# Optimization experiments

Measured on AMD Instinct MI355X. Metric: run time of the kernel, lower is better.

Reference implementation:

```python
import jax, jax.numpy as jnp
import numpy as np

N = 50000          # num nodes
E = 800000         # num edges
D = 128            # dim_in == embed_dim
MAX_NODES = 4      # hard-coded in SortConv.__init__
EPS = 1e-5


def setup_inputs() -> dict:
    key = jax.random.key(0)
    ks = jax.random.split(key, 16)
    inp = {
        'x': jax.random.normal(ks[0], (N, D), jnp.float32),
        'edge_index': jax.random.randint(ks[1], (2, E), 0, N, jnp.int32),
    }
    for i in range(2):
        o = 2 + 6 * i
        W = jax.random.normal(ks[o], (D, D), jnp.float32) * (2.0 / (D + D)) ** 0.5
        W = W / jnp.linalg.norm(W, axis=1, keepdims=True)   # reset_parameters row-normalization
        inp[f'W{i}'] = W
        inp[f'b{i}'] = jnp.zeros((D,), jnp.float32)
        inp[f'cw{i}'] = jax.random.normal(ks[o + 1], (MAX_NODES,), jnp.float32) * (2.0 / (MAX_NODES + 1)) ** 0.5
        inp[f'cb{i}'] = jnp.zeros((1,), jnp.float32)
        inp[f'a{i}'] = jax.random.uniform(ks[o + 2], (1,), jnp.float32, -1.0, 1.0)  # LinearCombination scalar
        inp[f'g{i}'] = jnp.ones((D,), jnp.float32)
        inp[f'be{i}'] = jnp.zeros((D,), jnp.float32)
        inp[f'blank{i}'] = jnp.zeros((D,), jnp.float32)      # learnable blank vector
    return inp


def sort_conv(x, edge_index, blank, W, b, cw, cb, a):
    n, d = x.shape
    e = edge_index.shape[1]
    src, dst = edge_index[0], edge_index[1]
    msgs = x[src]                                            # [E, D] raw messages (lin_project not applied to messages)
    order = jnp.argsort(dst)                                 # stable sort by destination (index_sort)
    dst_s = dst[order]
    counts = jax.ops.segment_sum(jnp.ones((e,), jnp.int32), dst, num_segments=n + 1)
    starts = jnp.concatenate([jnp.zeros((1,), jnp.int32), jnp.cumsum(counts)[:-1].astype(jnp.int32)])
    pos = jnp.arange(e, dtype=jnp.int32) - starts[dst_s]     # rank within each neighborhood
    slot = jnp.where(pos < MAX_NODES, pos, MAX_NODES)        # overflow edges -> trash slot (to_dense_batch truncation)
    dense = jnp.zeros((n + 1, MAX_NODES + 1, d), x.dtype).at[dst_s, slot].set(msgs[order])
    mask = jnp.zeros((n + 1, MAX_NODES + 1), bool).at[dst_s, slot].set(True)
    dense, mask = dense[:, :MAX_NODES], mask[:, :MAX_NODES]  # [N+1, 4, D], [N+1, 4]
    blank_p = W @ blank + b                                  # lin_project applied only to blank vector
    filled = dense + (~mask)[..., None].astype(x.dtype) * blank_p
    srt = jnp.sort(filled, axis=1)                           # per-feature sort over neighbor slots
    out = jnp.einsum('nmd,m->nd', srt, cw) + cb              # vector collapse: Linear(max_nodes, 1)
    node_out, blank_new = out[:-1], out[-1]                  # last row = all-blank graph -> new blank
    return a * x + node_out, a * blank + blank_new           # LinearCombination combine (num_repeats=1)


def batch_norm(h, g, be):
    mu = h.mean(0)
    var = h.var(0)
    return (h - mu) / jnp.sqrt(var + EPS) * g + be


def reference(x, edge_index, W0, b0, cw0, cb0, a0, g0, be0, blank0,
              W1, b1, cw1, cb1, a1, g1, be1, blank1):
    layers = [(W0, b0, cw0, cb0, a0, g0, be0, blank0),
              (W1, b1, cw1, cb1, a1, g1, be1, blank1)]
    for (W, b, cw, cb, a, g, be, blank) in layers:
        h, _ = sort_conv(x, edge_index, blank, W, b, cw, cb, a)
        h = batch_norm(h, g, be)
        x = x + h                                            # residual connection
    return x
```

## Files before the change

kernel.cpp:

```cpp
#include <hip/hip_runtime.h>
#include <climits>

constexpr int N_NODES = 50000;
constexpr int N_EDGES = 800000;
constexpr int DIM     = 128;
constexpr int DIM4    = DIM / 4;
constexpr float BN_EPS = 1e-5f;

constexpr int EMPTY = 0x7F7F7F7F;

constexpr int NC = 16;
constexpr int EC = 16;
constexpr int NODES_PER_NC = N_NODES / NC;
constexpr int EDGES_PER_EC = N_EDGES / EC;
constexpr int E4_PER_EC    = EDGES_PER_EC / 4;

constexpr int NODES_PER_ITER  = 8;
constexpr int CONV_ITERS      = 2;
constexpr int NODES_PER_BLOCK = NODES_PER_ITER * CONV_ITERS;
constexpr int CONV_GRID = N_NODES / NODES_PER_BLOCK;

constexpr int NBUCKETS = 64;

__device__ inline float4 f4min(float4 a, float4 b) {
    return make_float4(fminf(a.x,b.x), fminf(a.y,b.y), fminf(a.z,b.z), fminf(a.w,b.w));
}
__device__ inline float4 f4max(float4 a, float4 b) {
    return make_float4(fmaxf(a.x,b.x), fmaxf(a.y,b.y), fmaxf(a.z,b.z), fmaxf(a.w,b.w));
}
__device__ inline float4 f4add(float4 a, float4 b) {
    return make_float4(a.x+b.x, a.y+b.y, a.z+b.z, a.w+b.w);
}
__device__ inline float4 f4fma(float s, float4 v, float4 acc) {
    return make_float4(fmaf(s,v.x,acc.x), fmaf(s,v.y,acc.y), fmaf(s,v.z,acc.z), fmaf(s,v.w,acc.w));
}

__global__ __launch_bounds__(256)
void select_stageA_kernel(const int* __restrict__ dst,
                          int* __restrict__ tables) {
    __shared__ int slot[NODES_PER_NC * 4];
    const int nc = blockIdx.x & (NC - 1);
    const int ec = blockIdx.x >> 4;
    const int t  = threadIdx.x;

    for (int i = t; i < NODES_PER_NC * 4; i += 256) slot[i] = EMPTY;
    __syncthreads();

    const int r0 = nc * NODES_PER_NC;
    const int4* __restrict__ dst4 = (const int4*)dst;
    const int base4 = ec * E4_PER_EC;
    for (int i = t; i < E4_PER_EC; i += 256) {
        const int4 d = dst4[base4 + i];
        const int ebase = 4 * (base4 + i);
        #define TRY_INS(comp, off) {                                        \
            unsigned n_ = (unsigned)((comp) - r0);                          \
            if (n_ < (unsigned)NODES_PER_NC) {                              \
                int cur_ = ebase + (off);                                   \
                _Pragma("unroll")                                           \
                for (int j_ = 0; j_ < 4; ++j_) {                            \
                    int old_ = atomicMin(&slot[4 * n_ + j_], cur_);         \
                    if (old_ == EMPTY) break;                               \
                    cur_ = max(cur_, old_);                                 \
                } } }
        TRY_INS(d.x, 0); TRY_INS(d.y, 1); TRY_INS(d.z, 2); TRY_INS(d.w, 3);
        #undef TRY_INS
    }
    __syncthreads();

    int4* __restrict__ out = (int4*)tables + (size_t)ec * N_NODES + r0;
    const int4* __restrict__ sl4 = (const int4*)slot;
    for (int n = t; n < NODES_PER_NC; n += 256) out[n] = sl4[n];
}

__global__ void select_stageB_kernel(const int* __restrict__ tables,
                                     const int* __restrict__ src,
                                     int4* __restrict__ srcs4) {
    int v = blockIdx.x * blockDim.x + threadIdx.x;
    if (v >= N_NODES) return;

    int b0 = EMPTY, b1 = EMPTY, b2 = EMPTY, b3 = EMPTY;
    #pragma unroll
    for (int ec = 0; ec < EC; ++ec) {
        const int4 c = ((const int4*)tables)[(size_t)ec * N_NODES + v];
        #define INS(val) {                                          \
            int x_ = (val);                                         \
            if (x_ < b3) { b3 = x_;                                 \
                int tm;                                             \
                if (b3 < b2) { tm = b2; b2 = b3; b3 = tm; }         \
                if (b2 < b1) { tm = b1; b1 = b2; b2 = tm; }         \
                if (b1 < b0) { tm = b0; b0 = b1; b1 = tm; } } }
        INS(c.x); INS(c.y); INS(c.z); INS(c.w);
        #undef INS
    }
    int4 o;
    o.x = (b0 < N_EDGES) ? src[b0] : -1;
    o.y = (b1 < N_EDGES) ? src[b1] : -1;
    o.z = (b2 < N_EDGES) ? src[b2] : -1;
    o.w = (b3 < N_EDGES) ? src[b3] : -1;
    srcs4[v] = o;
}

__global__ void blank_proj_kernel(const float* __restrict__ W0, const float* __restrict__ b0,
                                  const float* __restrict__ bl0,
                                  const float* __restrict__ W1, const float* __restrict__ b1,
                                  const float* __restrict__ bl1,
                                  float* __restrict__ bp) {
    int l = blockIdx.x;
    int d = threadIdx.x;
    const float* W  = l ? W1  : W0;
    const float* b  = l ? b1  : b0;
    const float* bl = l ? bl1 : bl0;
    float s = 0.f;
    #pragma unroll 8
    for (int j = 0; j < DIM; ++j) s += W[d * DIM + j] * bl[j];
    bp[l * DIM + d] = s + b[d];
}

__global__ __launch_bounds__(256)
void conv_stats_kernel(const float* __restrict__ x,
                       const int4* __restrict__ srcs4,
                       const float* __restrict__ bp,
                       const float* __restrict__ cw,
                       const float* __restrict__ cb,
                       const float* __restrict__ a,
                       float* __restrict__ h,
                       float* __restrict__ stats_part) {
    const int t    = threadIdx.x;
    const int d4   = t & (DIM4 - 1);
    const int nsub = t >> 5;

    const float4* __restrict__ x4 = (const float4*)x;
    float4*       __restrict__ h4 = (float4*)h;

    const float aa = a[0];
    const float c0 = cw[0], c1 = cw[1], c2 = cw[2], c3 = cw[3];
    const float cbv = cb[0];
    const float4 bpv = ((const float4*)bp)[d4];

    const int v0 = blockIdx.x * NODES_PER_BLOCK + nsub;
    const int v1 = v0 + NODES_PER_ITER;

    const int4 s0 = srcs4[v0];
    const int4 s1 = srcs4[v1];

    float4 g00 = x4[(size_t)max(s0.x, 0) * DIM4 + d4];
    float4 g01 = x4[(size_t)max(s0.y, 0) * DIM4 + d4];
    float4 g02 = x4[(size_t)max(s0.z, 0) * DIM4 + d4];
    float4 g03 = x4[(size_t)max(s0.w, 0) * DIM4 + d4];
    float4 g10 = x4[(size_t)max(s1.x, 0) * DIM4 + d4];
    float4 g11 = x4[(size_t)max(s1.y, 0) * DIM4 + d4];
    float4 g12 = x4[(size_t)max(s1.z, 0) * DIM4 + d4];
    float4 g13 = x4[(size_t)max(s1.w, 0) * DIM4 + d4];
    float4 xv0 = x4[(size_t)v0 * DIM4 + d4];
    float4 xv1 = x4[(size_t)v1 * DIM4 + d4];

    float4 s  = make_float4(0.f, 0.f, 0.f, 0.f);
    float4 s2 = make_float4(0.f, 0.f, 0.f, 0.f);

    #define CSWAP4(p, q) { float4 lo = f4min(p, q); float4 hi = f4max(p, q); p = lo; q = hi; }
    {
        float4 m0 = (s0.x >= 0) ? g00 : bpv;
        float4 m1 = (s0.y >= 0) ? g01 : bpv;
        float4 m2 = (s0.z >= 0) ? g02 : bpv;
        float4 m3 = (s0.w >= 0) ? g03 : bpv;
        CSWAP4(m0, m1); CSWAP4(m2, m3); CSWAP4(m0, m2); CSWAP4(m1, m3); CSWAP4(m1, m2);
        float4 hv = make_float4(cbv, cbv, cbv, cbv);
        hv = f4fma(c0, m0, hv);
        hv = f4fma(c1, m1, hv);
        hv = f4fma(c2, m2, hv);
        hv = f4fma(c3, m3, hv);
        hv = f4fma(aa, xv0, hv);
        h4[(size_t)v0 * DIM4 + d4] = hv;
        s  = f4add(s, hv);
        s2 = f4add(s2, make_float4(hv.x*hv.x, hv.y*hv.y, hv.z*hv.z, hv.w*hv.w));
    }
    {
        float4 m0 = (s1.x >= 0) ? g10 : bpv;
        float4 m1 = (s1.y >= 0) ? g11 : bpv;
        float4 m2 = (s1.z >= 0) ? g12 : bpv;
        float4 m3 = (s1.w >= 0) ? g13 : bpv;
        CSWAP4(m0, m1); CSWAP4(m2, m3); CSWAP4(m0, m2); CSWAP4(m1, m3); CSWAP4(m1, m2);
        float4 hv = make_float4(cbv, cbv, cbv, cbv);
        hv = f4fma(c0, m0, hv);
        hv = f4fma(c1, m1, hv);
        hv = f4fma(c2, m2, hv);
        hv = f4fma(c3, m3, hv);
        hv = f4fma(aa, xv1, hv);
        h4[(size_t)v1 * DIM4 + d4] = hv;
        s  = f4add(s, hv);
        s2 = f4add(s2, make_float4(hv.x*hv.x, hv.y*hv.y, hv.z*hv.z, hv.w*hv.w));
    }
    #undef CSWAP4

    s.x  += __shfl_down(s.x, 32);  s.y  += __shfl_down(s.y, 32);
    s.z  += __shfl_down(s.z, 32);  s.w  += __shfl_down(s.w, 32);
    s2.x += __shfl_down(s2.x, 32); s2.y += __shfl_down(s2.y, 32);
    s2.z += __shfl_down(s2.z, 32); s2.w += __shfl_down(s2.w, 32);

    __shared__ float4 ls[4][32];
    __shared__ float4 ls2[4][32];
    const int wave = t >> 6;
    const int lane = t & 63;
    if (lane < 32) { ls[wave][lane] = s; ls2[wave][lane] = s2; }
    __syncthreads();
    if (t < 32) {
        float* bucket = stats_part + (size_t)(blockIdx.x & (NBUCKETS - 1)) * 256;
        float4 fs  = f4add(f4add(ls[0][t],  ls[1][t]),  f4add(ls[2][t],  ls[3][t]));
        float4 fs2 = f4add(f4add(ls2[0][t], ls2[1][t]), f4add(ls2[2][t], ls2[3][t]));
        atomicAdd(&bucket[4*t + 0], fs.x);
        atomicAdd(&bucket[4*t + 1], fs.y);
        atomicAdd(&bucket[4*t + 2], fs.z);
        atomicAdd(&bucket[4*t + 3], fs.w);
        atomicAdd(&bucket[DIM + 4*t + 0], fs2.x);
        atomicAdd(&bucket[DIM + 4*t + 1], fs2.y);
        atomicAdd(&bucket[DIM + 4*t + 2], fs2.z);
        atomicAdd(&bucket[DIM + 4*t + 3], fs2.w);
    }
}

__global__ void reduce_finalize_kernel(const float* __restrict__ stats_part,
                                       float* __restrict__ final) {
    __shared__ float acc[256];
    int t = threadIdx.x;
    float s = 0.f;
    #pragma unroll 8
    for (int k = 0; k < NBUCKETS; ++k) s += stats_part[k * 256 + t];
    acc[t] = s;
    __syncthreads();
    if (t < 128) {
        constexpr float invN = 1.0f / (float)N_NODES;
        float mu = acc[t] * invN;
        float iv = rsqrtf(acc[128 + t] * invN - mu * mu + BN_EPS);
        final[t]       = mu;
        final[128 + t] = iv;
    }
}

__global__ void bn_apply_kernel(const float* __restrict__ xin,
                                const float* __restrict__ h,
                                const float* __restrict__ final,
                                const float* __restrict__ g,
                                const float* __restrict__ be,
                                float* __restrict__ xout) {
    int idx = blockIdx.x * blockDim.x + threadIdx.x;
    constexpr int TOTAL4 = N_NODES * DIM4;
    if (idx >= TOTAL4) return;
    int d4 = idx & (DIM4 - 1);

    float4 mu = ((const float4*)final)[d4];
    float4 iv = ((const float4*)(final + DIM))[d4];
    float4 hv = ((const float4*)h)[idx];
    float4 xv = ((const float4*)xin)[idx];
    float4 gv = ((const float4*)g)[d4];
    float4 bv = ((const float4*)be)[d4];

    float4 o;
    o.x = xv.x + (hv.x - mu.x) * iv.x * gv.x + bv.x;
    o.y = xv.y + (hv.y - mu.y) * iv.y * gv.y + bv.y;
    o.z = xv.z + (hv.z - mu.z) * iv.z * gv.z + bv.z;
    o.w = xv.w + (hv.w - mu.w) * iv.w * gv.w + bv.w;
    ((float4*)xout)[idx] = o;
}

extern "C" void kernel_launch(void* const* d_in, const int* in_sizes, int n_in,
                              void* d_out, int out_size, void* d_ws, size_t ws_size,
                              hipStream_t stream) {
    const float* x0  = (const float*)d_in[0];
    const int*   ei  = (const int*)d_in[1];
    const int*   src = ei;
    const int*   dst = ei + N_EDGES;

    const float* W[2]; const float* b[2]; const float* cw[2]; const float* cb[2];
    const float* a[2]; const float* g[2]; const float* be[2]; const float* blank[2];
    for (int i = 0; i < 2; ++i) {
        int o = 2 + 8 * i;
        W[i]     = (const float*)d_in[o + 0];
        b[i]     = (const float*)d_in[o + 1];
        cw[i]    = (const float*)d_in[o + 2];
        cb[i]    = (const float*)d_in[o + 3];
        a[i]     = (const float*)d_in[o + 4];
        g[i]     = (const float*)d_in[o + 5];
        be[i]    = (const float*)d_in[o + 6];
        blank[i] = (const float*)d_in[o + 7];
    }

    char* ws = (char*)d_ws;
    int*   srcs       = (int*)ws;
    float* h          = (float*)(srcs + 4 * N_NODES);
    int*   tables     = (int*)h;
    float* stats_part = h + (size_t)N_NODES * DIM;
    float* final_     = stats_part + 2 * NBUCKETS * 256;
    float* bp         = final_ + 512;

    float* xout = (float*)d_out;

    hipMemsetAsync(stats_part, 0, 2 * NBUCKETS * 256 * sizeof(float), stream);

    select_stageA_kernel<<<NC * EC, 256, 0, stream>>>(dst, tables);
    select_stageB_kernel<<<(N_NODES + 255) / 256, 256, 0, stream>>>(
        tables, src, (int4*)srcs);

    blank_proj_kernel<<<2, DIM, 0, stream>>>(W[0], b[0], blank[0],
                                             W[1], b[1], blank[1], bp);

    for (int l = 0; l < 2; ++l) {
        const float* xin = (l == 0) ? x0 : xout;
        float* sp = stats_part + (size_t)l * NBUCKETS * 256;
        conv_stats_kernel<<<CONV_GRID, 256, 0, stream>>>(
            xin, (const int4*)srcs, bp + l * DIM, cw[l], cb[l], a[l], h, sp);
        reduce_finalize_kernel<<<1, 256, 0, stream>>>(sp, final_ + l * 256);
        bn_apply_kernel<<<(N_NODES * DIM4 + 255) / 256, 256, 0, stream>>>(
            xin, h, final_ + l * 256, g[l], be[l], xout);
    }
}
```

Before: 237.4 us.

## Fuse memset and blank projection into merge kernel, widen selection blocks

Folds the stats zeroing memset and the blank-vector projection kernel into the stage-B merge kernel as extra blocks, which removes two launches from the stream. Stage-A selection blocks grow from 256 to 1024 threads so more threads work on each shared-memory slot table. Stage-B also skips a table row early when its smallest entry cannot beat the current fourth-best. The larger blocks may lower occupancy and add contention on the shared-memory atomics.

```diff
diff --git a/kernel.cpp b/kernel.cpp
--- a/kernel.cpp
+++ b/kernel.cpp
@@ -14,6 +14,7 @@
 constexpr int NODES_PER_NC = N_NODES / NC;
 constexpr int EDGES_PER_EC = N_EDGES / EC;
 constexpr int E4_PER_EC    = EDGES_PER_EC / 4;
+constexpr int SEL_THREADS  = 1024;
 
 constexpr int NODES_PER_ITER  = 8;
 constexpr int CONV_ITERS      = 2;
@@ -21,6 +22,7 @@
 constexpr int CONV_GRID = N_NODES / NODES_PER_BLOCK;
 
 constexpr int NBUCKETS = 64;
+constexpr int NB_MERGE = (N_NODES + 255) / 256;
 
 __device__ inline float4 f4min(float4 a, float4 b) {
     return make_float4(fminf(a.x,b.x), fminf(a.y,b.y), fminf(a.z,b.z), fminf(a.w,b.w));
@@ -35,7 +37,7 @@
     return make_float4(fmaf(s,v.x,acc.x), fmaf(s,v.y,acc.y), fmaf(s,v.z,acc.z), fmaf(s,v.w,acc.w));
 }
 
-__global__ __launch_bounds__(256)
+__global__ __launch_bounds__(SEL_THREADS)
 void select_stageA_kernel(const int* __restrict__ dst,
                           int* __restrict__ tables) {
     __shared__ int slot[NODES_PER_NC * 4];
@@ -43,13 +45,13 @@
     const int ec = blockIdx.x >> 4;
     const int t  = threadIdx.x;
 
-    for (int i = t; i < NODES_PER_NC * 4; i += 256) slot[i] = EMPTY;
+    for (int i = t; i < NODES_PER_NC * 4; i += SEL_THREADS) slot[i] = EMPTY;
     __syncthreads();
 
     const int r0 = nc * NODES_PER_NC;
     const int4* __restrict__ dst4 = (const int4*)dst;
     const int base4 = ec * E4_PER_EC;
-    for (int i = t; i < E4_PER_EC; i += 256) {
+    for (int i = t; i < E4_PER_EC; i += SEL_THREADS) {
         const int4 d = dst4[base4 + i];
         const int ebase = 4 * (base4 + i);
         #define TRY_INS(comp, off) {                                        \
@@ -69,51 +71,62 @@
 
     int4* __restrict__ out = (int4*)tables + (size_t)ec * N_NODES + r0;
     const int4* __restrict__ sl4 = (const int4*)slot;
-    for (int n = t; n < NODES_PER_NC; n += 256) out[n] = sl4[n];
-}
-
-__global__ void select_stageB_kernel(const int* __restrict__ tables,
-                                     const int* __restrict__ src,
-                                     int4* __restrict__ srcs4) {
-    int v = blockIdx.x * blockDim.x + threadIdx.x;
+    for (int n = t; n < NODES_PER_NC; n += SEL_THREADS) out[n] = sl4[n];
+}
+
+__global__ __launch_bounds__(256)
+void select_stageB_kernel(const int* __restrict__ tables,
+                          const int* __restrict__ src,
+                          int4* __restrict__ srcs4,
+                          float* __restrict__ stats_part,
+                          const float* __restrict__ W0, const float* __restrict__ b0,
+                          const float* __restrict__ bl0,
+                          const float* __restrict__ W1, const float* __restrict__ b1,
+                          const float* __restrict__ bl1,
+                          float* __restrict__ bp) {
+    const int t = threadIdx.x;
+
+    if (blockIdx.x >= NB_MERGE) {
+        if (t < DIM) {
+            int l = blockIdx.x - NB_MERGE;
+            const float* W  = l ? W1  : W0;
+            const float* b  = l ? b1  : b0;
+            const float* bl = l ? bl1 : bl0;
+            float s = 0.f;
+            #pragma unroll 8
+            for (int j = 0; j < DIM; ++j) s += W[t * DIM + j] * bl[j];
+            bp[l * DIM + t] = s + b[t];
+        }
+        return;
+    }
+
+    const int gid = blockIdx.x * 256 + t;
+    if (gid < 2 * NBUCKETS * 256) stats_part[gid] = 0.f;
+
+    const int v = gid;
     if (v >= N_NODES) return;
 
-    int b0 = EMPTY, b1 = EMPTY, b2 = EMPTY, b3 = EMPTY;
+    int b0_ = EMPTY, b1_ = EMPTY, b2_ = EMPTY, b3_ = EMPTY;
     #pragma unroll
     for (int ec = 0; ec < EC; ++ec) {
         const int4 c = ((const int4*)tables)[(size_t)ec * N_NODES + v];
+        if (c.x >= b3_) continue;
         #define INS(val) {                                          \
             int x_ = (val);                                         \
-            if (x_ < b3) { b3 = x_;                                 \
+            if (x_ < b3_) { b3_ = x_;                               \
                 int tm;                                             \
-                if (b3 < b2) { tm = b2; b2 = b3; b3 = tm; }         \
-                if (b2 < b1) { tm = b1; b1 = b2; b2 = tm; }         \
-                if (b1 < b0) { tm = b0; b0 = b1; b1 = tm; } } }
+                if (b3_ < b2_) { tm = b2_; b2_ = b3_; b3_ = tm; }   \
+                if (b2_ < b1_) { tm = b1_; b1_ = b2_; b2_ = tm; }   \
+                if (b1_ < b0_) { tm = b0_; b0_ = b1_; b1_ = tm; } } }
         INS(c.x); INS(c.y); INS(c.z); INS(c.w);
         #undef INS
     }
     int4 o;
-    o.x = (b0 < N_EDGES) ? src[b0] : -1;
-    o.y = (b1 < N_EDGES) ? src[b1] : -1;
-    o.z = (b2 < N_EDGES) ? src[b2] : -1;
-    o.w = (b3 < N_EDGES) ? src[b3] : -1;
+    o.x = (b0_ < N_EDGES) ? src[b0_] : -1;
+    o.y = (b1_ < N_EDGES) ? src[b1_] : -1;
+    o.z = (b2_ < N_EDGES) ? src[b2_] : -1;
+    o.w = (b3_ < N_EDGES) ? src[b3_] : -1;
     srcs4[v] = o;
-}
-
-__global__ void blank_proj_kernel(const float* __restrict__ W0, const float* __restrict__ b0,
-                                  const float* __restrict__ bl0,
-                                  const float* __restrict__ W1, const float* __restrict__ b1,
-                                  const float* __restrict__ bl1,
-                                  float* __restrict__ bp) {
-    int l = blockIdx.x;
-    int d = threadIdx.x;
-    const float* W  = l ? W1  : W0;
-    const float* b  = l ? b1  : b0;
-    const float* bl = l ? bl1 : bl0;
-    float s = 0.f;
-    #pragma unroll 8
-    for (int j = 0; j < DIM; ++j) s += W[d * DIM + j] * bl[j];
-    bp[l * DIM + d] = s + b[d];
 }
 
 __global__ __launch_bounds__(256)
@@ -294,14 +307,10 @@
 
     float* xout = (float*)d_out;
 
-    hipMemsetAsync(stats_part, 0, 2 * NBUCKETS * 256 * sizeof(float), stream);
-
-    select_stageA_kernel<<<NC * EC, 256, 0, stream>>>(dst, tables);
-    select_stageB_kernel<<<(N_NODES + 255) / 256, 256, 0, stream>>>(
-        tables, src, (int4*)srcs);
-
-    blank_proj_kernel<<<2, DIM, 0, stream>>>(W[0], b[0], blank[0],
-                                             W[1], b[1], blank[1], bp);
+    select_stageA_kernel<<<NC * EC, SEL_THREADS, 0, stream>>>(dst, tables);
+    select_stageB_kernel<<<NB_MERGE + 2, 256, 0, stream>>>(
+        tables, src, (int4*)srcs, stats_part,
+        W[0], b[0], blank[0], W[1], b[1], blank[1], bp);
 
     for (int l = 0; l < 2; ++l) {
         const float* xin = (l == 0) ? x0 : xout;
```

New measurement: 207.9 us. -12.4%, faster.
